# Kernel optimization log

Hardware: AMD Instinct MI355X
Metric: run time of the kernel (lower is better)

Reference implementation:

```python
import jax, jax.numpy as jnp
import numpy as np
import math

DMODEL, DK, H, DFF = 1024, 64, 16, 4096
B, T = 2, 2048
EPS = 1e-5


def setup_inputs() -> dict:
    key = jax.random.key(0)
    ks = jax.random.split(key, 12)
    s = 0.02
    x = jax.random.normal(ks[0], (B, T, DMODEL), dtype=jnp.float32)
    # causal mask, broadcastable [1,1,T,T]; 0 -> masked (like masked_fill(mask==0, -inf))
    attention_mask = jnp.tril(jnp.ones((T, T), dtype=jnp.int32))[None, None]
    Wq = jax.random.normal(ks[1], (DMODEL, DK * H), dtype=jnp.float32) * s
    bq = jnp.zeros((DK * H,), jnp.float32)
    Wk = jax.random.normal(ks[2], (DMODEL, DK * H), dtype=jnp.float32) * s
    bk = jnp.zeros((DK * H,), jnp.float32)
    Wv = jax.random.normal(ks[3], (DMODEL, DMODEL), dtype=jnp.float32) * s
    bv = jnp.zeros((DMODEL,), jnp.float32)
    W1 = jax.random.normal(ks[4], (DMODEL, DFF), dtype=jnp.float32) * s
    b1 = jnp.zeros((DFF,), jnp.float32)
    W2 = jax.random.normal(ks[5], (DFF, DMODEL), dtype=jnp.float32) * s
    b2 = jnp.zeros((DMODEL,), jnp.float32)
    g1 = jnp.ones((DMODEL,), jnp.float32)
    be1 = jnp.zeros((DMODEL,), jnp.float32)
    g2 = jnp.ones((DMODEL,), jnp.float32)
    be2 = jnp.zeros((DMODEL,), jnp.float32)
    return dict(x=x, attention_mask=attention_mask, Wq=Wq, bq=bq, Wk=Wk, bk=bk,
                Wv=Wv, bv=bv, W1=W1, b1=b1, W2=W2, b2=b2,
                g1=g1, be1=be1, g2=g2, be2=be2)


def _layernorm(x, g, b):
    mu = jnp.mean(x, axis=-1, keepdims=True)
    var = jnp.mean(jnp.square(x - mu), axis=-1, keepdims=True)
    return (x - mu) * jax.lax.rsqrt(var + EPS) * g + b


def _split_heads(t, h):  # [B,T,h*d] -> [B,h,T,d]
    Bn, Tn, D = t.shape
    return t.reshape(Bn, Tn, h, D // h).transpose(0, 2, 1, 3)


def reference(x, attention_mask, Wq, bq, Wk, bk, Wv, bv, W1, b1, W2, b2, g1, be1, g2, be2):
    # multi-head self-attention (hand-rolled, matching torch module)
    q = _split_heads(x @ Wq + bq, H)                    # [B,h,T,dk]
    k = _split_heads(x @ Wk + bk, H)                    # [B,h,T,dk]
    v = _split_heads(x @ Wv + bv, H)                    # [B,h,T,dv]
    scores = jnp.einsum('bhqd,bhkd->bhqk', q, k) / math.sqrt(DK)
    scores = jnp.where(attention_mask == 0, -jnp.inf, scores)
    probs = jax.nn.softmax(scores, axis=-1)
    attn = jnp.einsum('bhqk,bhkd->bhqd', probs, v)      # [B,h,T,dv]
    attn = attn.transpose(0, 2, 1, 3).reshape(B, T, DMODEL)
    # double residual (dropout = identity in eval): x + dropout(attn) + attn
    x1 = _layernorm(x + 2.0 * attn, g1, be1)
    ff = jax.nn.relu(x1 @ W1 + b1) @ W2 + b2
    out = _layernorm(x1 + 2.0 * ff, g2, be2)
    return out
```

## Files before the change

### kernel.cpp

```cpp
#include <hip/hip_runtime.h>

#define DMODEL 1024
#define DKH 64
#define NH 16
#define DFF 4096
#define BB 2
#define TT 2048
#define ROWS (BB*TT)
#define QKVN (3*DMODEL)

typedef unsigned short ushort_t;
typedef __attribute__((ext_vector_type(8))) short s8v;
typedef __attribute__((ext_vector_type(4))) float f4v;
typedef __attribute__((ext_vector_type(4))) unsigned short us4v;

typedef const void __attribute__((address_space(1)))* GPTR;
typedef void __attribute__((address_space(3)))* SPTR;

__device__ __forceinline__ float bf2f(ushort_t u) {
  return __uint_as_float(((unsigned int)u) << 16);
}
__device__ __forceinline__ ushort_t f2bf(float f) {
  unsigned int u = __float_as_uint(f);
  u += 0x7fffu + ((u >> 16) & 1u);
  return (ushort_t)(u >> 16);
}
__device__ __forceinline__ void gload16(const void* g, void* l) {
  __builtin_amdgcn_global_load_lds((GPTR)g, (SPTR)l, 16, 0, 0);
}

__global__ __launch_bounds__(256) void cvt_f32_bf16(const float* __restrict__ in,
                                                    ushort_t* __restrict__ out, int n4) {
  int i = blockIdx.x * 256 + threadIdx.x;
  if (i >= n4) return;
  float4 v = ((const float4*)in)[i];
  us4v o;
  o.x = f2bf(v.x); o.y = f2bf(v.y); o.z = f2bf(v.z); o.w = f2bf(v.w);
  ((us4v*)out)[i] = o;
}

__global__ __launch_bounds__(256) void transpose_cvt(const float* __restrict__ in,
                                                     ushort_t* __restrict__ out, int R, int C) {
  __shared__ float tile[32][33];
  int bx = blockIdx.x * 32, by = blockIdx.y * 32;
  int tx = threadIdx.x, ty = threadIdx.y;
#pragma unroll
  for (int i = 0; i < 32; i += 8)
    tile[ty + i][tx] = in[(size_t)(by + ty + i) * C + bx + tx];
  __syncthreads();
#pragma unroll
  for (int i = 0; i < 32; i += 8)
    out[(size_t)(bx + ty + i) * R + by + tx] = f2bf(tile[tx][ty + i]);
}

__global__ void concat_bias(const float* __restrict__ a, const float* __restrict__ b,
                            const float* __restrict__ c, float* __restrict__ o) {
  int i = blockIdx.x * 256 + threadIdx.x;
  if (i < 1024) { o[i] = a[i]; o[1024 + i] = b[i]; o[2048 + i] = c[i]; }
}

__global__ __launch_bounds__(256) void vtrans(const ushort_t* __restrict__ QKV,
                                              ushort_t* __restrict__ VT) {
  __shared__ ushort_t tile[32][66];
  const int t0 = blockIdx.x * 32;
  const int bh = blockIdx.y;
  const int b = bh >> 4, h = bh & 15;
  const int tx = threadIdx.x, ty = threadIdx.y;
  const ushort_t* src = QKV + ((size_t)b * TT + t0) * QKVN + 2 * DMODEL + h * 64;
#pragma unroll
  for (int i = 0; i < 4; ++i) {
    int r = ty + i * 8;
    *(unsigned int*)&tile[r][tx * 2] = *(const unsigned int*)(src + (size_t)r * QKVN + tx * 2);
  }
  __syncthreads();
  unsigned int* dst = (unsigned int*)(VT + (size_t)bh * 64 * TT);
#pragma unroll
  for (int i = 0; i < 4; ++i) {
    int d = ty + i * 8 + (tx >> 4) * 32;
    int p = tx & 15;
    unsigned int lo = tile[2 * p][d], hi = tile[2 * p + 1][d];
    dst[(size_t)d * (TT / 2) + (t0 >> 1) + p] = lo | (hi << 16);
  }
}

template<int MODE>
__global__ __launch_bounds__(256) void gemm_m97(const ushort_t* __restrict__ A,
                                                const ushort_t* __restrict__ BT,
                                                const float* __restrict__ bias,
                                                ushort_t* __restrict__ C,
                                                int M, int N, int Kstride, int Kloop,
                                                int nbx, int tiles_per_k) {
  __shared__ __align__(16) ushort_t As[128 * 32];
  __shared__ __align__(16) ushort_t Bs[128 * 32];
  const int nwg = gridDim.x;
  const int wg = blockIdx.x;
  const int cpx = nwg >> 3;
  const int swz = (wg & 7) * cpx + (wg >> 3);
  const int ks = swz / tiles_per_k;
  const int tile = swz % tiles_per_k;
  const int bx = tile % nbx, by = tile / nbx;
  const int m0 = by * 128, n0 = bx * 128;
  const size_t kbase = (size_t)ks * Kloop;
  const int tid = threadIdx.x;
  const int w = tid >> 6, l = tid & 63, lr = l & 15, lg = l >> 4;
  const int wm = w >> 1, wn = w & 1;

  const int sr = tid >> 2;
  const int sch = tid & 3;

  auto stage = [&](int kt) {
#pragma unroll
    for (int s = 0; s < 2; ++s) {
      int row = s * 64 + sr;
      int scol = ((sch ^ (row & 3)) << 3);
      gload16(A + (size_t)(m0 + row) * Kstride + kbase + kt * 32 + scol,
              (char*)As + s * 4096 + tid * 16);
      gload16(BT + (size_t)(n0 + row) * Kstride + kbase + kt * 32 + scol,
              (char*)Bs + s * 4096 + tid * 16);
    }
  };

  auto ldA = [&](int m) -> s8v {
    int row = wm * 64 + m * 16 + lr;
    return *(const s8v*)((const char*)As + row * 64 + ((lg ^ (row & 3)) << 4));
  };
  auto ldB = [&](int n) -> s8v {
    int row = wn * 64 + n * 16 + lr;
    return *(const s8v*)((const char*)Bs + row * 64 + ((lg ^ (row & 3)) << 4));
  };

  f4v acc[4][4] = {};
  const int NT = Kloop >> 5;

  for (int kt = 0; kt < NT; ++kt) {
    stage(kt);
    __syncthreads();
    s8v af[4], bfr[4];
#pragma unroll
    for (int m = 0; m < 4; ++m) af[m] = ldA(m);
#pragma unroll
    for (int n = 0; n < 4; ++n) bfr[n] = ldB(n);
    __builtin_amdgcn_s_setprio(1);
#pragma unroll
    for (int m = 0; m < 4; ++m)
#pragma unroll
      for (int n = 0; n < 4; ++n)
        acc[m][n] = __builtin_amdgcn_mfma_f32_16x16x32_bf16(af[m], bfr[n], acc[m][n], 0, 0, 0);
    __builtin_amdgcn_s_setprio(0);
    __syncthreads();
  }

  ushort_t* Cp = (MODE == 2) ? (C + (size_t)ks * M * N) : C;
#pragma unroll
  for (int n = 0; n < 4; ++n) {
    int col = n0 + wn * 64 + n * 16 + lr;
    float bv = (MODE == 2) ? 0.f : bias[col];
#pragma unroll
    for (int m = 0; m < 4; ++m) {
      int row = m0 + wm * 64 + m * 16 + lg * 4;
#pragma unroll
      for (int j = 0; j < 4; ++j) {
        float v = acc[m][n][j] + bv;
        if (MODE == 1) v = fmaxf(v, 0.f);
        Cp[(size_t)(row + j) * N + col] = f2bf(v);
      }
    }
  }
}

__global__ __launch_bounds__(256) void attn_kernel(const ushort_t* __restrict__ QKV,
                                                   const ushort_t* __restrict__ VT,
                                                   ushort_t* __restrict__ O) {
  const int bh = blockIdx.x;
  const int byy = blockIdx.y;
  const int kk_ = byy >> 3, rr_ = byy & 7;
  const int qt = (kk_ & 1) ? (8 * kk_ + 7 - rr_) : (8 * kk_ + rr_);
  const int b = bh >> 4, h = bh & 15;
  const int nkt = qt + 1;
  const int tid = threadIdx.x;
  const int w = tid >> 6, l = tid & 63;
  const int lr = l & 15, lg = l >> 4;

  __shared__ __align__(16) ushort_t Ksh[2][64 * 64];
  __shared__ __align__(16) ushort_t Vsh[64 * 64];
  __shared__ __align__(16) ushort_t Psh[4][16 * 72];

  const size_t RS = QKVN;
  const ushort_t* Qb = QKV + (size_t)b * TT * RS + h * 64;
  const ushort_t* Kb = Qb + DMODEL;
  const ushort_t* Vb = VT + (size_t)bh * 64 * TT;

  s8v qf[2];
  {
    const ushort_t* qr = Qb + (size_t)(qt * 64 + w * 16 + lr) * RS + lg * 8;
    qf[0] = *(const s8v*)qr;
    qf[1] = *(const s8v*)(qr + 32);
  }
  f4v acc[4] = {};
  float lrow = 0.f;

  const int sr8 = l >> 3, sc = l & 7;

  auto stageK = [&](int kt, int buf) {
#pragma unroll
    for (int s = 0; s < 2; ++s) {
      int r = s * 32 + w * 8 + sr8;
      gload16(Kb + (size_t)(kt * 64 + r) * RS + ((sc ^ (r & 7)) << 3),
              (char*)&Ksh[buf][0] + (s * 32 + w * 8) * 128 + l * 16);
    }
  };
  auto stageV = [&](int kt) {
#pragma unroll
    for (int s = 0; s < 2; ++s) {
      int r = s * 32 + w * 8 + sr8;
      gload16(Vb + (size_t)r * TT + kt * 64 + ((sc ^ (r & 7)) << 3),
              (char*)&Vsh[0] + (s * 32 + w * 8) * 128 + l * 16);
    }
  };

  stageK(0, 0);
  for (int kt = 0; kt < nkt; ++kt) {
    const int cb = kt & 1;
    const bool last = (kt + 1 >= nkt);
    stageV(kt);
    if (!last) {
      stageK(kt + 1, cb ^ 1);
      asm volatile("s_waitcnt vmcnt(4)" ::: "memory");
    } else {
      asm volatile("s_waitcnt vmcnt(2)" ::: "memory");
    }
    __builtin_amdgcn_sched_barrier(0);
    __builtin_amdgcn_s_barrier();

    float ps = 0.f;
#pragma unroll
    for (int c = 0; c < 4; ++c) {
      f4v a = {};
      __builtin_amdgcn_s_setprio(1);
#pragma unroll
      for (int kk = 0; kk < 2; ++kk) {
        int rr = c * 16 + lr;
        int byte_ = (rr * 128 + kk * 64 + lg * 16) ^ ((rr & 7) << 4);
        s8v kf = *(const s8v*)((const char*)&Ksh[cb][0] + byte_);
        a = __builtin_amdgcn_mfma_f32_16x16x32_bf16(kf, qf[kk], a, 0, 0, 0);
      }
      __builtin_amdgcn_s_setprio(0);
      float e[4];
#pragma unroll
      for (int j = 0; j < 4; ++j) {
        e[j] = __expf(a[j] * 0.125f);
        if (last && (c * 16 + lg * 4 + j > w * 16 + lr)) e[j] = 0.f;
        ps += e[j];
      }
      unsigned int pk0, pk1;
      asm("v_cvt_pk_bf16_f32 %0, %1, %2" : "=v"(pk0) : "v"(e[0]), "v"(e[1]));
      asm("v_cvt_pk_bf16_f32 %0, %1, %2" : "=v"(pk1) : "v"(e[2]), "v"(e[3]));
      *(uint2*)((char*)&Psh[w][0] + lr * 144 + (c * 16 + lg * 4) * 2) = make_uint2(pk0, pk1);
    }
    s8v pa[2];
    pa[0] = *(const s8v*)((const char*)&Psh[w][0] + lr * 144 + lg * 16);
    pa[1] = *(const s8v*)((const char*)&Psh[w][0] + lr * 144 + 64 + lg * 16);

    if (!last) {
      asm volatile("s_waitcnt vmcnt(2)" ::: "memory");
    } else {
      asm volatile("s_waitcnt vmcnt(0)" ::: "memory");
    }
    __builtin_amdgcn_sched_barrier(0);
    __builtin_amdgcn_s_barrier();

    __builtin_amdgcn_s_setprio(1);
#pragma unroll
    for (int ks = 0; ks < 2; ++ks)
#pragma unroll
      for (int d = 0; d < 4; ++d) {
        int row = d * 16 + lr;
        int byte_ = (row * 128 + ks * 64 + lg * 16) ^ ((row & 7) << 4);
        s8v vf = *(const s8v*)((const char*)&Vsh[0] + byte_);
        acc[d] = __builtin_amdgcn_mfma_f32_16x16x32_bf16(pa[ks], vf, acc[d], 0, 0, 0);
      }
    __builtin_amdgcn_s_setprio(0);
    ps += __shfl_xor(ps, 16);
    ps += __shfl_xor(ps, 32);
    lrow += ps;
    __builtin_amdgcn_s_barrier();
  }

  float inv = 1.f / lrow;
  ushort_t* orow = O + ((size_t)b * TT + qt * 64 + w * 16) * DMODEL + h * 64;
#pragma unroll
  for (int j = 0; j < 4; ++j) {
    float invj = __shfl(inv, lg * 4 + j);
#pragma unroll
    for (int d = 0; d < 4; ++d)
      orow[(size_t)(lg * 4 + j) * DMODEL + d * 16 + lr] = f2bf(acc[d][j] * invj);
  }
}

__global__ __launch_bounds__(256) void ln_kernel(const float* __restrict__ aptr,
                                                 const ushort_t* __restrict__ bptr,
                                                 const float* __restrict__ g,
                                                 const float* __restrict__ be,
                                                 ushort_t* __restrict__ yptr) {
  const int row = blockIdx.x;
  const int t = threadIdx.x;
  const int w = t >> 6, l = t & 63;
  const size_t base = (size_t)row * DMODEL + t * 4;
  float v[4];
  us4v bb = *(const us4v*)(bptr + base);
  float4 xa = *(const float4*)(aptr + base);
  v[0] = xa.x + 2.f * bf2f(bb.x);
  v[1] = xa.y + 2.f * bf2f(bb.y);
  v[2] = xa.z + 2.f * bf2f(bb.z);
  v[3] = xa.w + 2.f * bf2f(bb.w);
  float s = v[0] + v[1] + v[2] + v[3];
  float s2 = v[0] * v[0] + v[1] * v[1] + v[2] * v[2] + v[3] * v[3];
#pragma unroll
  for (int off = 1; off <= 32; off <<= 1) {
    s += __shfl_xor(s, off);
    s2 += __shfl_xor(s2, off);
  }
  __shared__ float red[2][4];
  if (l == 0) { red[0][w] = s; red[1][w] = s2; }
  __syncthreads();
  s = red[0][0] + red[0][1] + red[0][2] + red[0][3];
  s2 = red[1][0] + red[1][1] + red[1][2] + red[1][3];
  const float mu = s * (1.f / 1024.f);
  const float var = s2 * (1.f / 1024.f) - mu * mu;
  const float rstd = rsqrtf(var + 1e-5f);
  float4 g4 = *(const float4*)(g + t * 4);
  float4 be4 = *(const float4*)(be + t * 4);
  us4v o;
  o.x = f2bf((v[0] - mu) * rstd * g4.x + be4.x);
  o.y = f2bf((v[1] - mu) * rstd * g4.y + be4.y);
  o.z = f2bf((v[2] - mu) * rstd * g4.z + be4.z);
  o.w = f2bf((v[3] - mu) * rstd * g4.w + be4.w);
  *(us4v*)(yptr + base) = o;
}

__global__ __launch_bounds__(256) void ln2_kernel(const ushort_t* __restrict__ x1,
                                                  const ushort_t* __restrict__ part,
                                                  const float* __restrict__ b2,
                                                  const float* __restrict__ g,
                                                  const float* __restrict__ be,
                                                  float* __restrict__ y) {
  const int row = blockIdx.x;
  const int t = threadIdx.x;
  const int w = t >> 6, l = t & 63;
  const size_t base = (size_t)row * DMODEL + t * 4;
  us4v xa = *(const us4v*)(x1 + base);
  float f[4] = {0.f, 0.f, 0.f, 0.f};
#pragma unroll
  for (int ks = 0; ks < 4; ++ks) {
    us4v p = *(const us4v*)(part + (size_t)ks * ROWS * DMODEL + base);
    f[0] += bf2f(p.x); f[1] += bf2f(p.y); f[2] += bf2f(p.z); f[3] += bf2f(p.w);
  }
  float4 b2v = *(const float4*)(b2 + t * 4);
  float v[4];
  v[0] = bf2f(xa.x) + 2.f * (f[0] + b2v.x);
  v[1] = bf2f(xa.y) + 2.f * (f[1] + b2v.y);
  v[2] = bf2f(xa.z) + 2.f * (f[2] + b2v.z);
  v[3] = bf2f(xa.w) + 2.f * (f[3] + b2v.w);
  float s = v[0] + v[1] + v[2] + v[3];
  float s2 = v[0] * v[0] + v[1] * v[1] + v[2] * v[2] + v[3] * v[3];
#pragma unroll
  for (int off = 1; off <= 32; off <<= 1) {
    s += __shfl_xor(s, off);
    s2 += __shfl_xor(s2, off);
  }
  __shared__ float red[2][4];
  if (l == 0) { red[0][w] = s; red[1][w] = s2; }
  __syncthreads();
  s = red[0][0] + red[0][1] + red[0][2] + red[0][3];
  s2 = red[1][0] + red[1][1] + red[1][2] + red[1][3];
  const float mu = s * (1.f / 1024.f);
  const float var = s2 * (1.f / 1024.f) - mu * mu;
  const float rstd = rsqrtf(var + 1e-5f);
  float4 g4 = *(const float4*)(g + t * 4);
  float4 be4 = *(const float4*)(be + t * 4);
  float4 o;
  o.x = (v[0] - mu) * rstd * g4.x + be4.x;
  o.y = (v[1] - mu) * rstd * g4.y + be4.y;
  o.z = (v[2] - mu) * rstd * g4.z + be4.z;
  o.w = (v[3] - mu) * rstd * g4.w + be4.w;
  *(float4*)(y + base) = o;
}

extern "C" void kernel_launch(void* const* d_in, const int* in_sizes, int n_in,
                              void* d_out, int out_size, void* d_ws, size_t ws_size,
                              hipStream_t stream) {
  const float* x   = (const float*)d_in[0];
  const float* Wq  = (const float*)d_in[2];
  const float* bq  = (const float*)d_in[3];
  const float* Wk  = (const float*)d_in[4];
  const float* bk  = (const float*)d_in[5];
  const float* Wv  = (const float*)d_in[6];
  const float* bv  = (const float*)d_in[7];
  const float* W1  = (const float*)d_in[8];
  const float* b1  = (const float*)d_in[9];
  const float* W2  = (const float*)d_in[10];
  const float* b2  = (const float*)d_in[11];
  const float* g1  = (const float*)d_in[12];
  const float* be1 = (const float*)d_in[13];
  const float* g2  = (const float*)d_in[14];
  const float* be2 = (const float*)d_in[15];
  float* out = (float*)d_out;

  char* ws = (char*)d_ws;
  size_t off = 0;
  auto alloc = [&](size_t bytes) {
    char* p = ws + off;
    off += (bytes + 255) & ~(size_t)255;
    return p;
  };
  ushort_t* xb    = (ushort_t*)alloc((size_t)ROWS * DMODEL * 2);
  ushort_t* WqkvT = (ushort_t*)alloc((size_t)QKVN * DMODEL * 2);
  ushort_t* W1T   = (ushort_t*)alloc((size_t)DFF * DMODEL * 2);
  ushort_t* W2T   = (ushort_t*)alloc((size_t)DMODEL * DFF * 2);
  ushort_t* QKV   = (ushort_t*)alloc((size_t)ROWS * QKVN * 2);
  ushort_t* VTb   = (ushort_t*)alloc((size_t)BB * NH * 64 * TT * 2);
  ushort_t* attnb = (ushort_t*)alloc((size_t)ROWS * DMODEL * 2);
  ushort_t* x1b   = (ushort_t*)alloc((size_t)ROWS * DMODEL * 2);
  ushort_t* H1b   = (ushort_t*)alloc((size_t)ROWS * DFF * 2);
  float* qkvb     = (float*)alloc(QKVN * 4);
  ushort_t* part  = QKV;
  (void)ws_size; (void)in_sizes; (void)n_in; (void)out_size;

  dim3 b256(256);
  dim3 tb(32, 8);
  cvt_f32_bf16<<<ROWS * DMODEL / 4 / 256, b256, 0, stream>>>(x, xb, ROWS * DMODEL / 4);
  transpose_cvt<<<dim3(32, 32), tb, 0, stream>>>(Wq, WqkvT, DMODEL, DMODEL);
  transpose_cvt<<<dim3(32, 32), tb, 0, stream>>>(Wk, WqkvT + DMODEL * DMODEL, DMODEL, DMODEL);
  transpose_cvt<<<dim3(32, 32), tb, 0, stream>>>(Wv, WqkvT + 2 * DMODEL * DMODEL, DMODEL, DMODEL);
  transpose_cvt<<<dim3(DFF / 32, DMODEL / 32), tb, 0, stream>>>(W1, W1T, DMODEL, DFF);
  transpose_cvt<<<dim3(DMODEL / 32, DFF / 32), tb, 0, stream>>>(W2, W2T, DFF, DMODEL);
  concat_bias<<<4, b256, 0, stream>>>(bq, bk, bv, qkvb);

  gemm_m97<0><<<dim3(768), b256, 0, stream>>>(xb, WqkvT, qkvb, QKV,
                                              ROWS, QKVN, DMODEL, DMODEL,
                                              QKVN / 128, 768);
  vtrans<<<dim3(TT / 32, BB * NH), tb, 0, stream>>>(QKV, VTb);
  attn_kernel<<<dim3(BB * NH, 32), b256, 0, stream>>>(QKV, VTb, attnb);
  ln_kernel<<<ROWS, b256, 0, stream>>>(x, attnb, g1, be1, x1b);
  gemm_m97<1><<<dim3(1024), b256, 0, stream>>>(x1b, W1T, b1, H1b,
                                               ROWS, DFF, DMODEL, DMODEL,
                                               DFF / 128, 1024);
  gemm_m97<2><<<dim3(1024), b256, 0, stream>>>(H1b, W2T, b2, part,
                                               ROWS, DMODEL, DFF, DFF / 4,
                                               DMODEL / 128, 256);
  ln2_kernel<<<ROWS, b256, 0, stream>>>(x1b, part, b2, g2, be2, out);
}
```

Measured before the change: 243.5 us.

## Triple-buffer GEMM LDS staging with async prefetch two tiles ahead

Replaces the single-buffer GEMM main loop, which loaded a K-tile and then waited on it, with a three-slot LDS ring. Tiles are prefetched two iterations ahead, and each step uses a vmcnt wait plus one barrier per iteration instead of two __syncthreads. The goal is to hide global-to-LDS load latency behind the MFMA work. The cost is triple the LDS footprint, about 48KB, which may lower occupancy. It also relies on hand-set waitcnt counts, so overlap with the buffer being written depends on the barrier placement.

```diff
diff --git a/kernel.cpp b/kernel.cpp
--- a/kernel.cpp
+++ b/kernel.cpp
@@ -84,14 +84,14 @@
 }
 
 template<int MODE>
-__global__ __launch_bounds__(256) void gemm_m97(const ushort_t* __restrict__ A,
-                                                const ushort_t* __restrict__ BT,
-                                                const float* __restrict__ bias,
-                                                ushort_t* __restrict__ C,
-                                                int M, int N, int Kstride, int Kloop,
-                                                int nbx, int tiles_per_k) {
-  __shared__ __align__(16) ushort_t As[128 * 32];
-  __shared__ __align__(16) ushort_t Bs[128 * 32];
+__global__ __launch_bounds__(256) void gemm_tb(const ushort_t* __restrict__ A,
+                                               const ushort_t* __restrict__ BT,
+                                               const float* __restrict__ bias,
+                                               ushort_t* __restrict__ C,
+                                               int M, int N, int Kstride, int Kloop,
+                                               int nbx, int tiles_per_k) {
+  __shared__ __align__(16) ushort_t As[3][128 * 32];
+  __shared__ __align__(16) ushort_t Bs[3][128 * 32];
   const int nwg = gridDim.x;
   const int wg = blockIdx.x;
   const int cpx = nwg >> 3;
@@ -108,38 +108,46 @@
   const int sr = tid >> 2;
   const int sch = tid & 3;
 
-  auto stage = [&](int kt) {
+  auto stage = [&](int kt, int buf) {
 #pragma unroll
     for (int s = 0; s < 2; ++s) {
       int row = s * 64 + sr;
       int scol = ((sch ^ (row & 3)) << 3);
       gload16(A + (size_t)(m0 + row) * Kstride + kbase + kt * 32 + scol,
-              (char*)As + s * 4096 + tid * 16);
+              (char*)&As[buf][0] + s * 4096 + tid * 16);
       gload16(BT + (size_t)(n0 + row) * Kstride + kbase + kt * 32 + scol,
-              (char*)Bs + s * 4096 + tid * 16);
-    }
-  };
-
-  auto ldA = [&](int m) -> s8v {
+              (char*)&Bs[buf][0] + s * 4096 + tid * 16);
+    }
+  };
+
+  auto ldA = [&](int buf, int m) -> s8v {
     int row = wm * 64 + m * 16 + lr;
-    return *(const s8v*)((const char*)As + row * 64 + ((lg ^ (row & 3)) << 4));
-  };
-  auto ldB = [&](int n) -> s8v {
+    return *(const s8v*)((const char*)&As[buf][0] + row * 64 + ((lg ^ (row & 3)) << 4));
+  };
+  auto ldB = [&](int buf, int n) -> s8v {
     int row = wn * 64 + n * 16 + lr;
-    return *(const s8v*)((const char*)Bs + row * 64 + ((lg ^ (row & 3)) << 4));
+    return *(const s8v*)((const char*)&Bs[buf][0] + row * 64 + ((lg ^ (row & 3)) << 4));
   };
 
   f4v acc[4][4] = {};
   const int NT = Kloop >> 5;
 
-  for (int kt = 0; kt < NT; ++kt) {
-    stage(kt);
-    __syncthreads();
+  stage(0, 0);
+  stage(1, 1);
+  for (int t = 0; t < NT; ++t) {
+    const int cb = t % 3;
+    if (t + 1 < NT) {
+      asm volatile("s_waitcnt vmcnt(4)" ::: "memory");
+    } else {
+      asm volatile("s_waitcnt vmcnt(0)" ::: "memory");
+    }
+    __builtin_amdgcn_sched_barrier(0);
+    __builtin_amdgcn_s_barrier();
     s8v af[4], bfr[4];
 #pragma unroll
-    for (int m = 0; m < 4; ++m) af[m] = ldA(m);
-#pragma unroll
-    for (int n = 0; n < 4; ++n) bfr[n] = ldB(n);
+    for (int m = 0; m < 4; ++m) af[m] = ldA(cb, m);
+#pragma unroll
+    for (int n = 0; n < 4; ++n) bfr[n] = ldB(cb, n);
     __builtin_amdgcn_s_setprio(1);
 #pragma unroll
     for (int m = 0; m < 4; ++m)
@@ -147,7 +155,7 @@
       for (int n = 0; n < 4; ++n)
         acc[m][n] = __builtin_amdgcn_mfma_f32_16x16x32_bf16(af[m], bfr[n], acc[m][n], 0, 0, 0);
     __builtin_amdgcn_s_setprio(0);
-    __syncthreads();
+    if (t + 2 < NT) stage(t + 2, (t + 2) % 3);
   }
 
   ushort_t* Cp = (MODE == 2) ? (C + (size_t)ks * M * N) : C;
@@ -436,17 +444,17 @@
   transpose_cvt<<<dim3(DMODEL / 32, DFF / 32), tb, 0, stream>>>(W2, W2T, DFF, DMODEL);
   concat_bias<<<4, b256, 0, stream>>>(bq, bk, bv, qkvb);
 
-  gemm_m97<0><<<dim3(768), b256, 0, stream>>>(xb, WqkvT, qkvb, QKV,
-                                              ROWS, QKVN, DMODEL, DMODEL,
-                                              QKVN / 128, 768);
+  gemm_tb<0><<<dim3(768), b256, 0, stream>>>(xb, WqkvT, qkvb, QKV,
+                                             ROWS, QKVN, DMODEL, DMODEL,
+                                             QKVN / 128, 768);
   vtrans<<<dim3(TT / 32, BB * NH), tb, 0, stream>>>(QKV, VTb);
   attn_kernel<<<dim3(BB * NH, 32), b256, 0, stream>>>(QKV, VTb, attnb);
   ln_kernel<<<ROWS, b256, 0, stream>>>(x, attnb, g1, be1, x1b);
-  gemm_m97<1><<<dim3(1024), b256, 0, stream>>>(x1b, W1T, b1, H1b,
-                                               ROWS, DFF, DMODEL, DMODEL,
-                                               DFF / 128, 1024);
-  gemm_m97<2><<<dim3(1024), b256, 0, stream>>>(H1b, W2T, b2, part,
-                                               ROWS, DMODEL, DFF, DFF / 4,
-                                               DMODEL / 128, 256);
+  gemm_tb<1><<<dim3(1024), b256, 0, stream>>>(x1b, W1T, b1, H1b,
+                                              ROWS, DFF, DMODEL, DMODEL,
+                                              DFF / 128, 1024);
+  gemm_tb<2><<<dim3(1024), b256, 0, stream>>>(H1b, W2T, b2, part,
+                                              ROWS, DMODEL, DFF, DFF / 4,
+                                              DMODEL / 128, 256);
   ln2_kernel<<<ROWS, b256, 0, stream>>>(x1b, part, b2, g2, be2, out);
 }
```

Result: faster. 238.0 us (-2.3%).
